# Performance work log

Measured on AMD Instinct MI355X. Metric: run time of the kernel, lower is better.

## Reference

```python
import jax, jax.numpy as jnp
import numpy as np

DN3D = ('NCDHW', 'OIDHW', 'NCDHW')

def conv_t3d(x, w, stride):
    # PyTorch ConvTranspose3d with padding=0: w is (C_in, C_out, k1,k2,k3).
    # Equivalent dilated conv: flip spatial dims, swap in/out channels,
    # lhs_dilation=stride, padding k-1 on each side.
    wf = jnp.flip(w, axis=(2, 3, 4)).transpose(1, 0, 2, 3, 4)  # (O, I, k, k, k)
    pad = [(k - 1, k - 1) for k in w.shape[2:]]
    dn = jax.lax.conv_dimension_numbers(x.shape, wf.shape, DN3D)
    return jax.lax.conv_general_dilated(x, wf, (1, 1, 1), pad,
                                        lhs_dilation=stride, dimension_numbers=dn)

def conv3d(x, w, stride, pad):
    dn = jax.lax.conv_dimension_numbers(x.shape, w.shape, DN3D)
    return jax.lax.conv_general_dilated(x, w, stride, [(pad, pad)] * 3,
                                        dimension_numbers=dn)

def setup_inputs() -> dict:
    key = jax.random.key(0)
    ks = jax.random.split(key, 7)
    out_ch, emb, p = 4, 256, 8
    B, T, D = 2, 8, 4  # batch, 4th spatial dim, coarse grid (input_size//patch_size)
    s = 0.05
    return {
        'x':  jax.random.normal(ks[0], (B, T, out_ch * emb, D, D, D), jnp.float32),
        'w1': jax.random.normal(ks[1], (out_ch * emb, out_ch * 2, p // 2, p // 2, p // 2), jnp.float32) * s,
        'b1': jax.random.normal(ks[2], (out_ch * 2,), jnp.float32) * s,
        'w2': jax.random.normal(ks[3], (out_ch * 2, out_ch * 2, 4, 4, 4), jnp.float32) * s,
        'b2': jax.random.normal(ks[4], (out_ch * 2,), jnp.float32) * s,
        'w3': jax.random.normal(ks[5], (out_ch, out_ch * 2, 4, 4, 4), jnp.float32) * s,
        'b3': jax.random.normal(ks[6], (out_ch,), jnp.float32) * s,
    }

def reference(x, w1, b1, w2, b2, w3, b3):
    # x: (B, D4, C_in, D1, D2, D3). All 4D kernels are size/stride 1 along D4,
    # so fold D4 into the batch and run 3D (de)convs.
    B, T, C, D, _, _ = x.shape
    h = x.reshape(B * T, C, D, D, D)
    bcast = lambda b: b[None, :, None, None, None]
    h = jnp.tanh(conv_t3d(h, w1, (4, 4, 4)) + bcast(b1))   # -> (BT, 8, 16,16,16)
    h = jnp.tanh(conv_t3d(h, w2, (4, 4, 4)) + bcast(b2))   # -> (BT, 8, 64,64,64)
    h = conv3d(h, w3, (2, 2, 2), 1) + bcast(b3)             # -> (BT, 4, 32,32,32)
    out = h.reshape(B, T, *h.shape[1:])                     # (B, D4, C, 32,32,32)
    return jnp.moveaxis(out, 1, -1)                         # (B, C, 32,32,32, D4)
```

## Files before the change

### kernel.cpp

```cpp
#include <hip/hip_runtime.h>
#include <cstdint>

typedef short bf16x8 __attribute__((ext_vector_type(8)));
typedef float f32x4 __attribute__((ext_vector_type(4)));

__device__ __forceinline__ unsigned short f2bf(float f) {
  unsigned u = __builtin_bit_cast(unsigned, f);
  u += 0x7fffu + ((u >> 16) & 1u);
  return (unsigned short)(u >> 16);
}
__device__ __forceinline__ float bflo(unsigned u) {
  return __builtin_bit_cast(float, u << 16);
}
__device__ __forceinline__ float bfhi(unsigned u) {
  return __builtin_bit_cast(float, u & 0xffff0000u);
}
__device__ __forceinline__ float fast_tanh(float x) {
  float e = __builtin_amdgcn_exp2f(x * 2.885390081777927f);
  return 1.0f - 2.0f * __builtin_amdgcn_rcpf(e + 1.0f);
}

#if __has_builtin(__builtin_amdgcn_fdot2_f32_bf16)
typedef __bf16 bf16x2 __attribute__((ext_vector_type(2)));
__device__ __forceinline__ float dot2bf(unsigned a, unsigned b, float c) {
  return __builtin_amdgcn_fdot2_f32_bf16(__builtin_bit_cast(bf16x2, a),
                                         __builtin_bit_cast(bf16x2, b), c,
                                         false);
}
#else
__device__ __forceinline__ float dot2bf(unsigned a, unsigned b, float c) {
  c = fmaf(bflo(a), bflo(b), c);
  c = fmaf(bfhi(a), bfhi(b), c);
  return c;
}
#endif

template <int ITERS>
__global__ __launch_bounds__(256) void k_stage1(const float* __restrict__ x,
                                                const float* __restrict__ w1,
                                                const float* __restrict__ w3,
                                                float* __restrict__ part,
                                                unsigned* __restrict__ wtab) {
  __shared__ __align__(16) char lds_raw[64 * 65 * 4];
  unsigned short* As = (unsigned short*)lds_raw;
  unsigned short* Bs = (unsigned short*)(lds_raw + 5120);
  float* Cs = (float*)lds_raw;

  const int tid = threadIdx.x;
  if (blockIdx.x == 0) {
    int l = tid << 2;
#pragma unroll
    for (int j = 0; j < 4; ++j) {
      int d = l + j;
      int slot = d & 3, chU = (d >> 2) & 1, kh = (d >> 3) & 3,
          kd = (d >> 5) & 3, cio = d >> 7;
      int co = (chU << 1) + (slot & 1);
      int kwb = (slot >> 1) << 1;
      int base = ((co << 3) + cio) * 64 + (kd << 4) + (kh << 2) + kwb;
      wtab[d] = (unsigned)f2bf(w3[base]) | ((unsigned)f2bf(w3[base + 1]) << 16);
    }
  }

  const int ks = blockIdx.x >> 7;
  const int bt = (blockIdx.x >> 3) & 15;
  const int co = blockIdx.x & 7;
  const int w = tid >> 6, lane = tid & 63, lm = lane & 15, q = lane >> 4;
  const int rrow = tid & 63, kgr = tid >> 6;

  f32x4 acc[4];
#pragma unroll
  for (int i = 0; i < 4; ++i) acc[i] = (f32x4){0.f, 0.f, 0.f, 0.f};

  const float* gA = x + (bt << 16) + ((size_t)(ks * ITERS * 32) << 6);
  const float* gB = w1 + (co << 6) + (size_t)(ks * ITERS * 32) * 512;

  float va[2][8], vb[2][8];
#define S1_LOAD(buf, it)                            \
  {                                                 \
    const int kb = (it) * 32 + (kgr << 3);          \
    _Pragma("unroll") for (int j = 0; j < 8; ++j) { \
      va[buf][j] = gA[((kb + j) << 6) | rrow];      \
      vb[buf][j] = gB[(kb + j) * 512 + rrow];       \
    }                                               \
  }
  S1_LOAD(0, 0);
#pragma unroll
  for (int it = 0; it < ITERS; ++it) {
    const int cur = it & 1;
    if (it + 1 < ITERS) S1_LOAD(cur ^ 1, it + 1);
    uint4 pa, pb;
    pa.x = f2bf(va[cur][0]) | ((unsigned)f2bf(va[cur][1]) << 16);
    pa.y = f2bf(va[cur][2]) | ((unsigned)f2bf(va[cur][3]) << 16);
    pa.z = f2bf(va[cur][4]) | ((unsigned)f2bf(va[cur][5]) << 16);
    pa.w = f2bf(va[cur][6]) | ((unsigned)f2bf(va[cur][7]) << 16);
    pb.x = f2bf(vb[cur][0]) | ((unsigned)f2bf(vb[cur][1]) << 16);
    pb.y = f2bf(vb[cur][2]) | ((unsigned)f2bf(vb[cur][3]) << 16);
    pb.z = f2bf(vb[cur][4]) | ((unsigned)f2bf(vb[cur][5]) << 16);
    pb.w = f2bf(vb[cur][6]) | ((unsigned)f2bf(vb[cur][7]) << 16);
    *(uint4*)&As[rrow * 40 + (kgr << 3)] = pa;
    *(uint4*)&Bs[rrow * 40 + (kgr << 3)] = pb;
    __syncthreads();
    bf16x8 a = *(const bf16x8*)&As[((w << 4) + lm) * 40 + (q << 3)];
#pragma unroll
    for (int nf = 0; nf < 4; ++nf) {
      bf16x8 b = *(const bf16x8*)&Bs[((nf << 4) + lm) * 40 + (q << 3)];
      acc[nf] = __builtin_amdgcn_mfma_f32_16x16x32_bf16(a, b, acc[nf], 0, 0, 0);
    }
    __syncthreads();
  }
#undef S1_LOAD
#pragma unroll
  for (int nf = 0; nf < 4; ++nf)
#pragma unroll
    for (int r = 0; r < 4; ++r) {
      int m = (w << 4) + (q << 2) + r;
      int n = (nf << 4) + lm;
      Cs[m * 65 + n] = acc[nf][r];
    }
  __syncthreads();
  float* dst = part + (((size_t)((ks << 4) + bt)) << 15) + co;
#pragma unroll
  for (int j = 0; j < 16; ++j) {
    int pos = (tid << 4) + j;
    int z = pos >> 8, y = (pos >> 4) & 15, xx = pos & 15;
    int m = ((z >> 2) << 4) + ((y >> 2) << 2) + (xx >> 2);
    int n = ((z & 3) << 4) + ((y & 3) << 2) + (xx & 3);
    dst[pos << 3] = Cs[m * 65 + n];
  }
}

__global__ __launch_bounds__(512) void k_stage23(
    const float* __restrict__ part, const float* __restrict__ w2,
    const float* __restrict__ b2, const float* __restrict__ b3,
    const float* __restrict__ b1, const unsigned* __restrict__ wtab,
    float* __restrict__ out, int nsplit) {
  __shared__ __align__(16) unsigned win_d[18 * 34 * 12];
  __shared__ __align__(16) unsigned h1p[6 * 240];
  __shared__ __align__(16) unsigned w2p[8 * 320];

  const int tid = threadIdx.x;
  const int bid = blockIdx.x;
  const int bt = bid >> 5;
  const int tile = bid & 31;
  const int tz = tile >> 3, ty = (tile >> 2) & 1, tx = tile & 3;
  const int Z0 = tz << 3, Y0 = ty << 4, X0 = tx << 3;
  const int Qz0 = (Z0 << 1) - 1, Qy0 = (Y0 << 1) - 1, Qx0 = (X0 << 1) - 1;
  const int Uz0 = (tz << 2) - 1, Uy0 = (ty << 3) - 1, Ux0 = (tx << 2) - 1;

  for (int l = tid; l < 2880; l += 512) {
    int ci = l & 7;
    int sp = l >> 3;
    int ux = sp % 6;
    int t1 = sp / 6;
    int uy = t1 % 10;
    int uz = t1 / 10;
    int gz = Uz0 + uz, gy = Uy0 + uy, gx = Ux0 + ux;
    float v = 0.f;
    if ((unsigned)gz < 16u && (unsigned)gy < 16u && (unsigned)gx < 16u) {
      const float* p =
          part + (((size_t)bt << 12) + (gz << 8) + (gy << 4) + gx) * 8 + ci;
      float s = b1[ci];
      for (int sg = 0; sg < nsplit; ++sg) s += p[(size_t)sg << 19];
      v = fast_tanh(s);
    }
    ((unsigned short*)h1p)[uz * 480 + uy * 48 + (ux << 3) + ci] = f2bf(v);
  }
  for (int l = tid; l < 2048; l += 512) {
    int j = l & 3, kx = (l >> 2) & 3, kzy = (l >> 4) & 15, cio = l >> 8;
    int kpos = (kzy << 2) + kx;
    float w0 = w2[(((j << 1) << 3) + cio) * 64 + kpos];
    float w1v = w2[((((j << 1) + 1) << 3) + cio) * 64 + kpos];
    w2p[cio * 320 + kzy * 20 + (kx << 2) + j] =
        (unsigned)f2bf(w0) | ((unsigned)f2bf(w1v) << 16);
  }

  float acc[2][4];
#pragma unroll
  for (int a = 0; a < 2; ++a)
#pragma unroll
    for (int i = 0; i < 4; ++i) acc[a][i] = 0.f;

  const int xh = tid & 1, yq = (tid >> 1) & 15, zq = (tid >> 5) & 7;
  const int chS = __builtin_amdgcn_readfirstlane(tid >> 8);

  for (int cio = 0; cio < 8; ++cio) {
    __syncthreads();
    const float b2c = b2[cio];
    for (int u = tid; u < 1224; u += 512) {
      int wz = u / 68;
      int rem = u - wz * 68;
      int wy = rem >> 1;
      int half = rem & 1;
      unsigned* wrow = win_d + (wz * 34 + wy) * 12;
      int qz = Qz0 + wz, qy = Qy0 + wy;
      if ((unsigned)qz < 64u && (unsigned)qy < 64u) {
        int kz = qz & 3, ky = qy & 3;
        int uzp = (qz >> 2) - Uz0, uyp = (qy >> 2) - Uy0;
        const unsigned* w2b = w2p + cio * 320 + ((kz << 2) + ky) * 20;
        uint4 wv[4];
#pragma unroll
        for (int kx = 0; kx < 4; ++kx) wv[kx] = *(const uint4*)(w2b + (kx << 2));
        const unsigned* h1b = h1p + uzp * 240 + uyp * 24;
#define DOT8(hc, kx)                                               \
  dot2bf((hc).w, wv[kx].w,                                         \
         dot2bf((hc).z, wv[kx].z,                                  \
                dot2bf((hc).y, wv[kx].y, dot2bf((hc).x, wv[kx].x, b2c))))
        if (half == 0) {
          uint4 h0 = *(const uint4*)(h1b);
          uint4 h1c = *(const uint4*)(h1b + 4);
          uint4 h2c = *(const uint4*)(h1b + 8);
          float vals[8];
          vals[0] = (Qx0 >= 0) ? fast_tanh(DOT8(h0, 3)) : 0.f;
#pragma unroll
          for (int kx = 0; kx < 4; ++kx) vals[1 + kx] = fast_tanh(DOT8(h1c, kx));
#pragma unroll
          for (int kx = 0; kx < 3; ++kx) vals[5 + kx] = fast_tanh(DOT8(h2c, kx));
          uint4 s0;
          s0.x = f2bf(vals[0]) | ((unsigned)f2bf(vals[1]) << 16);
          s0.y = f2bf(vals[2]) | ((unsigned)f2bf(vals[3]) << 16);
          s0.z = f2bf(vals[4]) | ((unsigned)f2bf(vals[5]) << 16);
          s0.w = f2bf(vals[6]) | ((unsigned)f2bf(vals[7]) << 16);
          *(uint4*)wrow = s0;
        } else {
          uint4 h2c = *(const uint4*)(h1b + 8);
          uint4 h3 = *(const uint4*)(h1b + 12);
          uint4 h4 = *(const uint4*)(h1b + 16);
          uint4 h5 = *(const uint4*)(h1b + 20);
          float vals[10];
          vals[0] = fast_tanh(DOT8(h2c, 3));
#pragma unroll
          for (int kx = 0; kx < 4; ++kx) vals[1 + kx] = fast_tanh(DOT8(h3, kx));
#pragma unroll
          for (int kx = 0; kx < 4; ++kx) vals[5 + kx] = fast_tanh(DOT8(h4, kx));
          vals[9] = (Qx0 + 17 < 64) ? fast_tanh(DOT8(h5, 0)) : 0.f;
          uint4 s1;
          s1.x = f2bf(vals[0]) | ((unsigned)f2bf(vals[1]) << 16);
          s1.y = f2bf(vals[2]) | ((unsigned)f2bf(vals[3]) << 16);
          s1.z = f2bf(vals[4]) | ((unsigned)f2bf(vals[5]) << 16);
          s1.w = f2bf(vals[6]) | ((unsigned)f2bf(vals[7]) << 16);
          *(uint4*)(wrow + 4) = s1;
          wrow[8] = f2bf(vals[8]) | ((unsigned)f2bf(vals[9]) << 16);
        }
#undef DOT8
      } else {
        uint4 zz;
        zz.x = zz.y = zz.z = zz.w = 0u;
        if (half == 0) {
          *(uint4*)wrow = zz;
        } else {
          *(uint4*)(wrow + 4) = zz;
          wrow[8] = 0u;
        }
      }
    }
    __syncthreads();
#pragma unroll
    for (int kd = 0; kd < 4; ++kd) {
      int wz = (zq << 1) + kd;
#pragma unroll
      for (int kh = 0; kh < 4; ++kh) {
        int wy = (yq << 1) + kh;
        const unsigned* rowp = win_d + (wz * 34 + wy) * 12 + (xh << 2);
        uint4 rv = *(const uint4*)rowp;
        unsigned r4 = rowp[4];
        unsigned r[5] = {rv.x, rv.y, rv.z, rv.w, r4};
        const uint4 wv =
            *(const uint4*)&wtab[((((cio << 4) + (kd << 2) + kh) << 1) + chS)
                                 << 2];
        unsigned wA[2] = {wv.x, wv.y};
        unsigned wB[2] = {wv.z, wv.w};
#pragma unroll
        for (int cc = 0; cc < 2; ++cc) {
#pragma unroll
          for (int i = 0; i < 4; ++i) {
            float a0 = dot2bf(r[i], wA[cc], acc[cc][i]);
            acc[cc][i] = dot2bf(r[i + 1], wB[cc], a0);
          }
        }
      }
    }
  }
  const int ch = tid >> 8;
  const int b = bt >> 3, t8 = bt & 7;
  const int z = Z0 + zq;
  const int y = Y0 + yq;
#pragma unroll
  for (int cc = 0; cc < 2; ++cc) {
    int c4 = (ch << 1) + cc;
    float bias = b3[c4];
#pragma unroll
    for (int i = 0; i < 4; ++i) {
      int xx = X0 + (xh << 2) + i;
      out[(((((b << 2) + c4) * 32 + z) * 32 + y) * 32 + xx) << 3 | t8] =
          acc[cc][i] + bias;
    }
  }
}

extern "C" void kernel_launch(void* const* d_in, const int* in_sizes, int n_in,
                              void* d_out, int out_size, void* d_ws,
                              size_t ws_size, hipStream_t stream) {
  (void)in_sizes; (void)n_in; (void)out_size;
  const float* x = (const float*)d_in[0];
  const float* w1 = (const float*)d_in[1];
  const float* b1 = (const float*)d_in[2];
  const float* w2 = (const float*)d_in[3];
  const float* b2 = (const float*)d_in[4];
  const float* w3 = (const float*)d_in[5];
  const float* b3 = (const float*)d_in[6];
  float* out = (float*)d_out;
  float* part = (float*)d_ws;

  const size_t plane = (size_t)16 * 8 * 4096;
  int nsplit = (ws_size >= 2 * plane * 4 + 4096) ? 2 : 1;
  unsigned* wtab = (unsigned*)(part + (size_t)nsplit * plane);

  if (nsplit == 2)
    k_stage1<16><<<dim3(256), dim3(256), 0, stream>>>(x, w1, w3, part, wtab);
  else
    k_stage1<32><<<dim3(128), dim3(256), 0, stream>>>(x, w1, w3, part, wtab);
  k_stage23<<<dim3(512), dim3(512), 0, stream>>>(part, w2, b2, b3, b1, wtab,
                                                 out, nsplit);
}
```

Measured before the change: 156.9 us.

## Switch stage23 to fp16 dot2 and double-buffer the LDS window

Replaces the bf16 packing and bf16 dot2 with fp16: packing now uses cvt_pkrtz and the dot products use fdot2 on half pairs, which cuts the software rounding cost of f2bf. The LDS window is double-buffered across input channels, which removes one __syncthreads per iteration. Border zero-fill is hoisted out of the channel loop into a single prologue pass. In exchange the window uses twice the LDS, which may lower occupancy, and fp16 has less range than bf16.

```diff
diff --git a/kernel.cpp b/kernel.cpp
--- a/kernel.cpp
+++ b/kernel.cpp
@@ -3,34 +3,32 @@
 
 typedef short bf16x8 __attribute__((ext_vector_type(8)));
 typedef float f32x4 __attribute__((ext_vector_type(4)));
+typedef _Float16 half2_t __attribute__((ext_vector_type(2)));
 
 __device__ __forceinline__ unsigned short f2bf(float f) {
   unsigned u = __builtin_bit_cast(unsigned, f);
   u += 0x7fffu + ((u >> 16) & 1u);
   return (unsigned short)(u >> 16);
 }
-__device__ __forceinline__ float bflo(unsigned u) {
-  return __builtin_bit_cast(float, u << 16);
-}
-__device__ __forceinline__ float bfhi(unsigned u) {
-  return __builtin_bit_cast(float, u & 0xffff0000u);
+__device__ __forceinline__ unsigned pkh2(float a, float b) {
+  return __builtin_bit_cast(unsigned, __builtin_amdgcn_cvt_pkrtz(a, b));
 }
 __device__ __forceinline__ float fast_tanh(float x) {
   float e = __builtin_amdgcn_exp2f(x * 2.885390081777927f);
   return 1.0f - 2.0f * __builtin_amdgcn_rcpf(e + 1.0f);
 }
 
-#if __has_builtin(__builtin_amdgcn_fdot2_f32_bf16)
-typedef __bf16 bf16x2 __attribute__((ext_vector_type(2)));
-__device__ __forceinline__ float dot2bf(unsigned a, unsigned b, float c) {
-  return __builtin_amdgcn_fdot2_f32_bf16(__builtin_bit_cast(bf16x2, a),
-                                         __builtin_bit_cast(bf16x2, b), c,
-                                         false);
+#if __has_builtin(__builtin_amdgcn_fdot2)
+__device__ __forceinline__ float dot2h(unsigned a, unsigned b, float c) {
+  return __builtin_amdgcn_fdot2(__builtin_bit_cast(half2_t, a),
+                                __builtin_bit_cast(half2_t, b), c, false);
 }
 #else
-__device__ __forceinline__ float dot2bf(unsigned a, unsigned b, float c) {
-  c = fmaf(bflo(a), bflo(b), c);
-  c = fmaf(bfhi(a), bfhi(b), c);
+__device__ __forceinline__ float dot2h(unsigned a, unsigned b, float c) {
+  half2_t av = __builtin_bit_cast(half2_t, a);
+  half2_t bv = __builtin_bit_cast(half2_t, b);
+  c = fmaf((float)av.x, (float)bv.x, c);
+  c = fmaf((float)av.y, (float)bv.y, c);
   return c;
 }
 #endif
@@ -57,7 +55,7 @@
       int co = (chU << 1) + (slot & 1);
       int kwb = (slot >> 1) << 1;
       int base = ((co << 3) + cio) * 64 + (kd << 4) + (kh << 2) + kwb;
-      wtab[d] = (unsigned)f2bf(w3[base]) | ((unsigned)f2bf(w3[base + 1]) << 16);
+      wtab[d] = pkh2(w3[base], w3[base + 1]);
     }
   }
 
@@ -134,7 +132,7 @@
     const float* __restrict__ b2, const float* __restrict__ b3,
     const float* __restrict__ b1, const unsigned* __restrict__ wtab,
     float* __restrict__ out, int nsplit) {
-  __shared__ __align__(16) unsigned win_d[18 * 34 * 12];
+  __shared__ __align__(16) unsigned win_d[2][18 * 34 * 12];
   __shared__ __align__(16) unsigned h1p[6 * 240];
   __shared__ __align__(16) unsigned w2p[8 * 320];
 
@@ -163,16 +161,36 @@
       for (int sg = 0; sg < nsplit; ++sg) s += p[(size_t)sg << 19];
       v = fast_tanh(s);
     }
-    ((unsigned short*)h1p)[uz * 480 + uy * 48 + (ux << 3) + ci] = f2bf(v);
+    ((_Float16*)h1p)[uz * 480 + uy * 48 + (ux << 3) + ci] = (_Float16)v;
   }
   for (int l = tid; l < 2048; l += 512) {
     int j = l & 3, kx = (l >> 2) & 3, kzy = (l >> 4) & 15, cio = l >> 8;
     int kpos = (kzy << 2) + kx;
     float w0 = w2[(((j << 1) << 3) + cio) * 64 + kpos];
     float w1v = w2[((((j << 1) + 1) << 3) + cio) * 64 + kpos];
-    w2p[cio * 320 + kzy * 20 + (kx << 2) + j] =
-        (unsigned)f2bf(w0) | ((unsigned)f2bf(w1v) << 16);
-  }
+    w2p[cio * 320 + kzy * 20 + (kx << 2) + j] = pkh2(w0, w1v);
+  }
+  for (int u = tid; u < 1224; u += 512) {
+    int wz = u / 68;
+    int rem = u - wz * 68;
+    int wy = rem >> 1;
+    int half = rem & 1;
+    int qz = Qz0 + wz, qy = Qy0 + wy;
+    if ((unsigned)qz < 64u && (unsigned)qy < 64u) continue;
+    uint4 zz;
+    zz.x = zz.y = zz.z = zz.w = 0u;
+#pragma unroll
+    for (int bsel = 0; bsel < 2; ++bsel) {
+      unsigned* wrow = win_d[bsel] + (wz * 34 + wy) * 12;
+      if (half == 0) {
+        *(uint4*)wrow = zz;
+      } else {
+        *(uint4*)(wrow + 4) = zz;
+        wrow[8] = 0u;
+      }
+    }
+  }
+  __syncthreads();
 
   float acc[2][4];
 #pragma unroll
@@ -184,74 +202,64 @@
   const int chS = __builtin_amdgcn_readfirstlane(tid >> 8);
 
   for (int cio = 0; cio < 8; ++cio) {
-    __syncthreads();
+    unsigned* wbuf = win_d[cio & 1];
     const float b2c = b2[cio];
     for (int u = tid; u < 1224; u += 512) {
       int wz = u / 68;
       int rem = u - wz * 68;
       int wy = rem >> 1;
       int half = rem & 1;
-      unsigned* wrow = win_d + (wz * 34 + wy) * 12;
       int qz = Qz0 + wz, qy = Qy0 + wy;
-      if ((unsigned)qz < 64u && (unsigned)qy < 64u) {
-        int kz = qz & 3, ky = qy & 3;
-        int uzp = (qz >> 2) - Uz0, uyp = (qy >> 2) - Uy0;
-        const unsigned* w2b = w2p + cio * 320 + ((kz << 2) + ky) * 20;
-        uint4 wv[4];
-#pragma unroll
-        for (int kx = 0; kx < 4; ++kx) wv[kx] = *(const uint4*)(w2b + (kx << 2));
-        const unsigned* h1b = h1p + uzp * 240 + uyp * 24;
-#define DOT8(hc, kx)                                               \
-  dot2bf((hc).w, wv[kx].w,                                         \
-         dot2bf((hc).z, wv[kx].z,                                  \
-                dot2bf((hc).y, wv[kx].y, dot2bf((hc).x, wv[kx].x, b2c))))
-        if (half == 0) {
-          uint4 h0 = *(const uint4*)(h1b);
-          uint4 h1c = *(const uint4*)(h1b + 4);
-          uint4 h2c = *(const uint4*)(h1b + 8);
-          float vals[8];
-          vals[0] = (Qx0 >= 0) ? fast_tanh(DOT8(h0, 3)) : 0.f;
-#pragma unroll
-          for (int kx = 0; kx < 4; ++kx) vals[1 + kx] = fast_tanh(DOT8(h1c, kx));
-#pragma unroll
-          for (int kx = 0; kx < 3; ++kx) vals[5 + kx] = fast_tanh(DOT8(h2c, kx));
-          uint4 s0;
-          s0.x = f2bf(vals[0]) | ((unsigned)f2bf(vals[1]) << 16);
-          s0.y = f2bf(vals[2]) | ((unsigned)f2bf(vals[3]) << 16);
-          s0.z = f2bf(vals[4]) | ((unsigned)f2bf(vals[5]) << 16);
-          s0.w = f2bf(vals[6]) | ((unsigned)f2bf(vals[7]) << 16);
-          *(uint4*)wrow = s0;
-        } else {
-          uint4 h2c = *(const uint4*)(h1b + 8);
-          uint4 h3 = *(const uint4*)(h1b + 12);
-          uint4 h4 = *(const uint4*)(h1b + 16);
-          uint4 h5 = *(const uint4*)(h1b + 20);
-          float vals[10];
-          vals[0] = fast_tanh(DOT8(h2c, 3));
-#pragma unroll
-          for (int kx = 0; kx < 4; ++kx) vals[1 + kx] = fast_tanh(DOT8(h3, kx));
-#pragma unroll
-          for (int kx = 0; kx < 4; ++kx) vals[5 + kx] = fast_tanh(DOT8(h4, kx));
-          vals[9] = (Qx0 + 17 < 64) ? fast_tanh(DOT8(h5, 0)) : 0.f;
-          uint4 s1;
-          s1.x = f2bf(vals[0]) | ((unsigned)f2bf(vals[1]) << 16);
-          s1.y = f2bf(vals[2]) | ((unsigned)f2bf(vals[3]) << 16);
-          s1.z = f2bf(vals[4]) | ((unsigned)f2bf(vals[5]) << 16);
-          s1.w = f2bf(vals[6]) | ((unsigned)f2bf(vals[7]) << 16);
-          *(uint4*)(wrow + 4) = s1;
-          wrow[8] = f2bf(vals[8]) | ((unsigned)f2bf(vals[9]) << 16);
-        }
+      if (!((unsigned)qz < 64u && (unsigned)qy < 64u)) continue;
+      unsigned* wrow = wbuf + (wz * 34 + wy) * 12;
+      int kz = qz & 3, ky = qy & 3;
+      int uzp = (qz >> 2) - Uz0, uyp = (qy >> 2) - Uy0;
+      const unsigned* w2b = w2p + cio * 320 + ((kz << 2) + ky) * 20;
+      uint4 wv[4];
+#pragma unroll
+      for (int kx = 0; kx < 4; ++kx) wv[kx] = *(const uint4*)(w2b + (kx << 2));
+      const unsigned* h1b = h1p + uzp * 240 + uyp * 24;
+#define DOT8(hc, kx)                                            \
+  dot2h((hc).w, wv[kx].w,                                       \
+        dot2h((hc).z, wv[kx].z,                                 \
+              dot2h((hc).y, wv[kx].y, dot2h((hc).x, wv[kx].x, b2c))))
+      if (half == 0) {
+        uint4 h0 = *(const uint4*)(h1b);
+        uint4 h1c = *(const uint4*)(h1b + 4);
+        uint4 h2c = *(const uint4*)(h1b + 8);
+        float vals[8];
+        vals[0] = (Qx0 >= 0) ? fast_tanh(DOT8(h0, 3)) : 0.f;
+#pragma unroll
+        for (int kx = 0; kx < 4; ++kx) vals[1 + kx] = fast_tanh(DOT8(h1c, kx));
+#pragma unroll
+        for (int kx = 0; kx < 3; ++kx) vals[5 + kx] = fast_tanh(DOT8(h2c, kx));
+        uint4 s0;
+        s0.x = pkh2(vals[0], vals[1]);
+        s0.y = pkh2(vals[2], vals[3]);
+        s0.z = pkh2(vals[4], vals[5]);
+        s0.w = pkh2(vals[6], vals[7]);
+        *(uint4*)wrow = s0;
+      } else {
+        uint4 h2c = *(const uint4*)(h1b + 8);
+        uint4 h3 = *(const uint4*)(h1b + 12);
+        uint4 h4 = *(const uint4*)(h1b + 16);
+        uint4 h5 = *(const uint4*)(h1b + 20);
+        float vals[10];
+        vals[0] = fast_tanh(DOT8(h2c, 3));
+#pragma unroll
+        for (int kx = 0; kx < 4; ++kx) vals[1 + kx] = fast_tanh(DOT8(h3, kx));
+#pragma unroll
+        for (int kx = 0; kx < 4; ++kx) vals[5 + kx] = fast_tanh(DOT8(h4, kx));
+        vals[9] = (Qx0 + 17 < 64) ? fast_tanh(DOT8(h5, 0)) : 0.f;
+        uint4 s1;
+        s1.x = pkh2(vals[0], vals[1]);
+        s1.y = pkh2(vals[2], vals[3]);
+        s1.z = pkh2(vals[4], vals[5]);
+        s1.w = pkh2(vals[6], vals[7]);
+        *(uint4*)(wrow + 4) = s1;
+        wrow[8] = pkh2(vals[8], vals[9]);
+      }
 #undef DOT8
-      } else {
-        uint4 zz;
-        zz.x = zz.y = zz.z = zz.w = 0u;
-        if (half == 0) {
-          *(uint4*)wrow = zz;
-        } else {
-          *(uint4*)(wrow + 4) = zz;
-          wrow[8] = 0u;
-        }
-      }
     }
     __syncthreads();
 #pragma unroll
@@ -260,7 +268,7 @@
 #pragma unroll
       for (int kh = 0; kh < 4; ++kh) {
         int wy = (yq << 1) + kh;
-        const unsigned* rowp = win_d + (wz * 34 + wy) * 12 + (xh << 2);
+        const unsigned* rowp = wbuf + (wz * 34 + wy) * 12 + (xh << 2);
         uint4 rv = *(const uint4*)rowp;
         unsigned r4 = rowp[4];
         unsigned r[5] = {rv.x, rv.y, rv.z, rv.w, r4};
@@ -273,8 +281,8 @@
         for (int cc = 0; cc < 2; ++cc) {
 #pragma unroll
           for (int i = 0; i < 4; ++i) {
-            float a0 = dot2bf(r[i], wA[cc], acc[cc][i]);
-            acc[cc][i] = dot2bf(r[i + 1], wB[cc], a0);
+            float a0 = dot2h(r[i], wA[cc], acc[cc][i]);
+            acc[cc][i] = dot2h(r[i + 1], wB[cc], a0);
           }
         }
       }
```

New measurement: 151.1 us. 3.7% less time.
